# Kernel tuning notes

Measured on AMD Instinct MI355X. Metric: run time of the kernel, lower is better.

Reference implementation:

```python
import jax, jax.numpy as jnp
import numpy as np

EPS = 1e-6
N_HEAD = 16

def alibi_slopes(n_head):
    # standard ALiBi geometric slopes for power-of-2 head counts
    start = 2.0 ** (-8.0 / n_head)
    return (start ** np.arange(1, n_head + 1)).astype(np.float32)

def rsig(x):
    # rational sigmoid sigma(x) = 0.5 * (x / (|x| + 1) + 1)
    return 0.5 * (x / (jnp.abs(x) + 1.0) + 1.0)

def mr_norm(x, w):
    # RationalMR: x / (mean(|x|) + eps) * weight
    return x / (jnp.mean(jnp.abs(x), axis=-1, keepdims=True) + EPS) * w


def setup_inputs() -> dict:
    key = jax.random.key(0)
    ks = jax.random.split(key, 6)
    d_model, d_ffn = 1024, 4096
    B, T = 1, 2048
    x = jax.random.normal(ks[0], (B, T, d_model), dtype=jnp.float32)
    s = 0.02
    w_qkv = jax.random.normal(ks[1], (3 * d_model, d_model), dtype=jnp.float32) * s
    w_out = jax.random.normal(ks[2], (d_model, d_model), dtype=jnp.float32) * s
    w_merged = jax.random.normal(ks[3], (2 * d_ffn, d_model), dtype=jnp.float32) * s
    w3 = jax.random.normal(ks[4], (d_model, d_ffn), dtype=jnp.float32) * s
    norm1_w = jnp.ones((d_model,), dtype=jnp.float32)
    norm2_w = jnp.ones((d_model,), dtype=jnp.float32)
    return {"x": x, "w_qkv": w_qkv, "w_out": w_out, "w_merged": w_merged,
            "w3": w3, "norm1_w": norm1_w, "norm2_w": norm2_w}


def reference(x, w_qkv, w_out, w_merged, w3, norm1_w, norm2_w):
    B, T, C = x.shape
    H = N_HEAD
    D = C // H
    scale = 1.0 / jnp.sqrt(jnp.float32(D))

    # --- attention sub-block ---
    h = mr_norm(x, norm1_w)
    qkv = (h @ w_qkv.T).reshape(B, T, 3, H, D).transpose(2, 0, 3, 1, 4)  # [3,B,H,T,D]
    q, k, v = qkv[0], qkv[1], qkv[2]
    scores = jnp.einsum('bhtd,bhsd->bhts', q, k) * scale  # [B,H,T,T]
    pos = jnp.arange(T)
    rel = jnp.abs(pos[:, None] - pos[None, :]).astype(jnp.float32)
    slopes = jnp.asarray(alibi_slopes(H))
    scores = scores - rel[None, None] * slopes[None, :, None, None]
    causal = pos[None, :] > pos[:, None]  # mask j > i
    scores = jnp.where(causal[None, None], jnp.float32(-10000.0), scores)
    # rational softmax: sigma(s)^4 / (sum sigma(s)^4 + eps)
    p4 = rsig(scores) ** 4
    probs = p4 / (jnp.sum(p4, axis=-1, keepdims=True) + EPS)
    attn = jnp.einsum('bhts,bhsd->bhtd', probs, v)  # [B,H,T,D]
    attn = attn.transpose(0, 2, 1, 3).reshape(B, T, C)
    x = x + attn @ w_out.T

    # --- FFN sub-block (rational SwiGLU) ---
    h2 = mr_norm(x, norm2_w)
    merged = h2 @ w_merged.T
    gate, val = jnp.split(merged, 2, axis=-1)
    hidden = gate * rsig(gate) * val
    x = x + hidden @ w3.T
    return x
```

## Files before the change

### kernel.cpp

```cpp
#include <hip/hip_runtime.h>
#include <hip/hip_bf16.h>
#include <stdint.h>

typedef unsigned int u32;
typedef unsigned short u16;
typedef __attribute__((ext_vector_type(8))) short bf16x8;
typedef __attribute__((ext_vector_type(4))) float f32x4;

#define MFMA(a, b, c) __builtin_amdgcn_mfma_f32_16x16x32_bf16(a, b, c, 0, 0, 0)

__device__ __forceinline__ u16 f2bf(float f) {
  u32 u = __float_as_uint(f);
  return (u16)((u + 0x7FFFu + ((u >> 16) & 1u)) >> 16);
}
__device__ __forceinline__ float bf2f(u16 h) {
  return __uint_as_float(((u32)h) << 16);
}
__device__ __forceinline__ float rsig_fast(float sc) {
  return 0.5f + 0.5f * sc * __builtin_amdgcn_rcpf(fabsf(sc) + 1.f);
}
__device__ __forceinline__ void async16(void* lds, const void* g) {
  __builtin_amdgcn_global_load_lds((const __attribute__((address_space(1))) u32*)g,
                                   (__attribute__((address_space(3))) u32*)lds, 16, 0, 0);
}

__global__ __launch_bounds__(256) void to_bf16(const float* __restrict__ src,
                                               u16* __restrict__ dst) {
  const size_t i = (size_t)blockIdx.x * 256 + threadIdx.x;
  const float4 a = ((const float4*)src)[2 * i];
  const float4 b = ((const float4*)src)[2 * i + 1];
  ushort4 o0, o1;
  o0.x = f2bf(a.x); o0.y = f2bf(a.y); o0.z = f2bf(a.z); o0.w = f2bf(a.w);
  o1.x = f2bf(b.x); o1.y = f2bf(b.y); o1.z = f2bf(b.z); o1.w = f2bf(b.w);
  ((ushort4*)dst)[2 * i] = o0;
  ((ushort4*)dst)[2 * i + 1] = o1;
}

__global__ __launch_bounds__(256) void mrnorm(const float* __restrict__ x,
                                              const float* __restrict__ wg,
                                              u16* __restrict__ out) {
  const int row = blockIdx.x;
  const int tid = threadIdx.x;
  const float4 v = ((const float4*)(x + (size_t)row * 1024))[tid];
  float s = fabsf(v.x) + fabsf(v.y) + fabsf(v.z) + fabsf(v.w);
#pragma unroll
  for (int off = 1; off < 64; off <<= 1) s += __shfl_xor(s, off);
  __shared__ float red[4];
  if ((tid & 63) == 0) red[tid >> 6] = s;
  __syncthreads();
  const float inv = 1.f / ((red[0] + red[1] + red[2] + red[3]) * (1.f / 1024.f) + 1e-6f);
  const float4 g = ((const float4*)wg)[tid];
  ushort4 o;
  o.x = f2bf(v.x * inv * g.x);
  o.y = f2bf(v.y * inv * g.y);
  o.z = f2bf(v.z * inv * g.z);
  o.w = f2bf(v.w * inv * g.w);
  ((ushort4*)out)[(size_t)row * 256 + tid] = o;
}

template <int EPI, bool DBUF>
__global__ __launch_bounds__(256) void gemm_bt(const u16* __restrict__ A, int lda,
                                               const u16* __restrict__ B, int ldb,
                                               void* __restrict__ C,
                                               const float* __restrict__ resid,
                                               int M, int N, int K) {
  __shared__ __align__(16) u16 As[(DBUF ? 2 : 1) * 128 * 64];
  __shared__ __align__(16) u16 Bs[(DBUF ? 2 : 1) * 128 * 64];
  const int tid = threadIdx.x;
  const int lane = tid & 63;
  const int w = tid >> 6;
  const int wr = (w >> 1) << 6;
  const int wc = (w & 1) << 6;
  const int nbn = N >> 7;
  const int m0 = (blockIdx.x / nbn) << 7;
  const int n0 = (blockIdx.x % nbn) << 7;
  const int l15 = lane & 15;
  const int lhi = lane >> 4;
  A += (size_t)blockIdx.y * K;
  B += (size_t)blockIdx.y * K;

  f32x4 acc[4][4] = {};

  auto stage = [&](int buf, int k0) {
#pragma unroll
    for (int p = 0; p < 4; ++p) {
      const int c = p * 256 + tid;
      const int row = c >> 3;
      const int cb = (c & 7) << 4;
      const int src = cb ^ ((row & 7) << 4);
      async16((char*)As + buf * 16384 + c * 16,
              (const char*)A + ((size_t)(m0 + row) * lda + k0) * 2 + src);
      async16((char*)Bs + buf * 16384 + c * 16,
              (const char*)B + ((size_t)(n0 + row) * ldb + k0) * 2 + src);
    }
  };
  auto compute = [&](int buf) {
#pragma unroll
    for (int kk = 0; kk < 2; ++kk) {
      bf16x8 af[4], bfr[4];
#pragma unroll
      for (int m = 0; m < 4; ++m) {
        const int row = wr + (m << 4) + l15;
        const int off = row * 128 + (((kk << 6) + (lhi << 4)) ^ ((row & 7) << 4));
        af[m] = *(const bf16x8*)((const char*)As + buf * 16384 + off);
      }
#pragma unroll
      for (int n = 0; n < 4; ++n) {
        const int row = wc + (n << 4) + l15;
        const int off = row * 128 + (((kk << 6) + (lhi << 4)) ^ ((row & 7) << 4));
        bfr[n] = *(const bf16x8*)((const char*)Bs + buf * 16384 + off);
      }
#pragma unroll
      for (int m = 0; m < 4; ++m)
#pragma unroll
        for (int n = 0; n < 4; ++n)
          acc[m][n] = MFMA(af[m], bfr[n], acc[m][n]);
    }
  };

  if (DBUF) {
    stage(0, 0);
    __syncthreads();
    int cur = 0;
    for (int k0 = 0; k0 < K; k0 += 64) {
      if (k0 + 64 < K) stage(cur ^ 1, k0 + 64);
      compute(cur);
      __syncthreads();
      cur ^= 1;
    }
  } else {
    for (int k0 = 0; k0 < K; k0 += 64) {
      stage(0, k0);
      __syncthreads();
      compute(0);
      __syncthreads();
    }
  }

  u16* Cp = (u16*)C + (size_t)blockIdx.y * M * N;
#pragma unroll
  for (int m = 0; m < 4; ++m) {
#pragma unroll
    for (int n = 0; n < 4; ++n) {
      const int col = n0 + wc + (n << 4) + l15;
#pragma unroll
      for (int r = 0; r < 4; ++r) {
        const int row = m0 + wr + (m << 4) + (lhi << 2) + r;
        const float v = acc[m][n][r];
        if (EPI == 0) {
          Cp[(size_t)row * N + col] = f2bf(v);
        } else {
          const size_t idx = (size_t)row * N + col;
          ((float*)C)[idx] = resid[idx] + v;
        }
      }
    }
  }
}

__global__ __launch_bounds__(256) void splitk_reduce(const u16* __restrict__ part,
                                                     const float* __restrict__ resid,
                                                     float* __restrict__ out) {
  const size_t i = ((size_t)blockIdx.x * 256 + threadIdx.x) * 8;
  const float4 r0 = *(const float4*)(resid + i);
  const float4 r1 = *(const float4*)(resid + i + 4);
  float acc[8] = {r0.x, r0.y, r0.z, r0.w, r1.x, r1.y, r1.z, r1.w};
#pragma unroll
  for (int c = 0; c < 4; ++c) {
    const uint4 p = *(const uint4*)(part + (size_t)c * 2097152 + i);
    const u16* ps = (const u16*)&p;
#pragma unroll
    for (int j = 0; j < 8; ++j) acc[j] += bf2f(ps[j]);
  }
  float4 o0 = {acc[0], acc[1], acc[2], acc[3]};
  float4 o1 = {acc[4], acc[5], acc[6], acc[7]};
  *(float4*)(out + i) = o0;
  *(float4*)(out + i + 4) = o1;
}

__global__ __launch_bounds__(256) void transpose_v(const u16* __restrict__ qkv,
                                                   u16* __restrict__ vt) {
  __shared__ __align__(16) u16 tile[64][72];
  const int head = blockIdx.x >> 5;
  const int t0 = (blockIdx.x & 31) << 6;
  const int tid = threadIdx.x;
  const int row = tid >> 2;
  const int cb = (tid & 3) << 4;
  const u16* src = qkv + (size_t)(t0 + row) * 3072 + 2048 + head * 64 + cb;
  *(uint4*)&tile[row][cb] = *(const uint4*)src;
  *(uint4*)&tile[row][cb + 8] = *(const uint4*)(src + 8);
  __syncthreads();
  u16 buf[16];
#pragma unroll
  for (int j = 0; j < 16; ++j) buf[j] = tile[cb + j][row];
  u16* dst = vt + (size_t)(head * 64 + row) * 2048 + t0 + cb;
  *(uint4*)dst = *(const uint4*)&buf[0];
  *(uint4*)(dst + 8) = *(const uint4*)&buf[8];
}

__global__ __launch_bounds__(256) void attn_part(const u16* __restrict__ qkv,
                                                 const u16* __restrict__ vt,
                                                 u16* __restrict__ pnum,
                                                 float* __restrict__ pden) {
  const int id = blockIdx.x;
  const int head = id & 15;
  const int rem = id >> 4;
  int a, g;
  if (rem < 32)      { a = 3; g = rem; }
  else if (rem < 56) { a = 2; g = rem - 32; }
  else if (rem < 72) { a = 1; g = rem - 56; }
  else               { a = 0; g = rem - 72; }
  const int qb = (a << 3) + g / (a + 1);
  const int c = g - (g / (a + 1)) * (a + 1);
  const int slot = head * 80 + ((a * (a + 1)) << 2) + (qb - (a << 3)) * (a + 1) + c;

  __shared__ __align__(16) u16 Ks[2][64 * 64];
  __shared__ __align__(16) u16 Vs[2][64 * 64];
  __shared__ __align__(16) u16 QP[4][16 * 64];
  const int tid = threadIdx.x;
  const int lane = tid & 63;
  const int w = tid >> 6;
  const int l15 = lane & 15;
  const int lhi = lane >> 4;
  const int qbase = qb << 6;
  const float slope = exp2f(-0.5f * (float)(head + 1));

  auto stageKV = [&](int buf, int s0) {
#pragma unroll
    for (int p = 0; p < 2; ++p) {
      const int cc = p * 256 + tid;
      const int row = cc >> 3;
      const int cb = (cc & 7) << 4;
      const int src = cb ^ ((row & 7) << 4);
      async16((char*)Ks[buf] + cc * 16,
              (const char*)qkv + ((size_t)(s0 + row) * 3072 + 1024 + head * 64) * 2 + src);
      async16((char*)Vs[buf] + cc * 16,
              (const char*)vt + ((size_t)(head * 64 + row) * 2048 + s0) * 2 + src);
    }
  };

  const int sfirst = c << 9;
  const int smax = min(qbase, sfirst + 448);
#pragma unroll
  for (int p = 0; p < 2; ++p) {
    const int cc = p * 256 + tid;
    const int row = cc >> 3;
    const int cb = (cc & 7) << 4;
    const int src = cb ^ ((row & 7) << 4);
    async16((char*)QP + cc * 16,
            (const char*)qkv + ((size_t)(qbase + row) * 3072 + head * 64) * 2 + src);
  }
  stageKV(0, sfirst);
  __syncthreads();

  bf16x8 qf[2];
#pragma unroll
  for (int kk = 0; kk < 2; ++kk) {
    const int row = (w << 4) + l15;
    const int off = row * 128 + (((kk << 6) + (lhi << 4)) ^ ((row & 7) << 4));
    qf[kk] = *(const bf16x8*)((const char*)QP + off);
  }

  f32x4 oacc[4] = {};
  float rs[4] = {0.f, 0.f, 0.f, 0.f};
  u16* pw = (u16*)QP[w];
  int cur = 0;

  for (int s0 = sfirst; s0 <= smax; s0 += 64) {
    if (s0 + 64 <= smax) stageKV(cur ^ 1, s0 + 64);
    const char* Kc = (const char*)Ks[cur];
    const char* Vc = (const char*)Vs[cur];

    bf16x8 kf[4][2];
#pragma unroll
    for (int bb = 0; bb < 4; ++bb)
#pragma unroll
      for (int kk = 0; kk < 2; ++kk) {
        const int row = (bb << 4) + l15;
        const int off = row * 128 + (((kk << 6) + (lhi << 4)) ^ ((row & 7) << 4));
        kf[bb][kk] = *(const bf16x8*)(Kc + off);
      }
    f32x4 sa[4];
#pragma unroll
    for (int bb = 0; bb < 4; ++bb) {
      f32x4 z = {0.f, 0.f, 0.f, 0.f};
      z = MFMA(qf[0], kf[bb][0], z);
      sa[bb] = MFMA(qf[1], kf[bb][1], z);
    }
#pragma unroll
    for (int bb = 0; bb < 4; ++bb) {
      const int s_abs = s0 + (bb << 4) + l15;
#pragma unroll
      for (int r = 0; r < 4; ++r) {
        const int prow = (lhi << 2) + r;
        const int q_abs = qbase + (w << 4) + prow;
        float p4 = 0.f;
        if (s_abs <= q_abs) {
          const float sc = sa[bb][r] * 0.125f - slope * (float)(q_abs - s_abs);
          const float t = rsig_fast(sc);
          const float t2 = t * t;
          p4 = t2 * t2;
        }
        rs[r] += p4;
        const int pcol2 = ((bb << 4) + l15) << 1;
        const int poff = prow * 128 + (pcol2 ^ ((prow & 7) << 4));
        *(u16*)((char*)pw + poff) = f2bf(p4);
      }
    }
    bf16x8 pf[2];
#pragma unroll
    for (int kk = 0; kk < 2; ++kk) {
      const int row = l15;
      const int off = row * 128 + (((kk << 6) + (lhi << 4)) ^ ((row & 7) << 4));
      pf[kk] = *(const bf16x8*)((const char*)pw + off);
    }
#pragma unroll
    for (int db = 0; db < 4; ++db) {
#pragma unroll
      for (int kk = 0; kk < 2; ++kk) {
        const int row = (db << 4) + l15;
        const int off = row * 128 + (((kk << 6) + (lhi << 4)) ^ ((row & 7) << 4));
        const bf16x8 vf = *(const bf16x8*)(Vc + off);
        oacc[db] = MFMA(pf[kk], vf, oacc[db]);
      }
    }
    __syncthreads();
    cur ^= 1;
  }

#pragma unroll
  for (int r = 0; r < 4; ++r) {
    float v = rs[r];
    v += __shfl_xor(v, 1);
    v += __shfl_xor(v, 2);
    v += __shfl_xor(v, 4);
    v += __shfl_xor(v, 8);
    rs[r] = v;
  }
  if (l15 == 0) {
#pragma unroll
    for (int r = 0; r < 4; ++r)
      pden[(size_t)slot * 64 + (w << 4) + (lhi << 2) + r] = rs[r];
  }
  __syncthreads();
#pragma unroll
  for (int db = 0; db < 4; ++db)
#pragma unroll
    for (int r = 0; r < 4; ++r)
      pw[((lhi << 2) + r) * 64 + (db << 4) + l15] = f2bf(oacc[db][r]);
  __syncthreads();
  {
    const int row = lane >> 2;
    const int cb = (lane & 3) << 4;
    const u16* s = pw + row * 64 + cb;
    const uint4 d0 = *(const uint4*)s;
    const uint4 d1 = *(const uint4*)(s + 8);
    u16* dst = pnum + (size_t)slot * 4096 + ((w << 4) + row) * 64 + cb;
    *(uint4*)dst = d0;
    *(uint4*)(dst + 8) = d1;
  }
}

__global__ __launch_bounds__(256) void attn_merge(const u16* __restrict__ pnum,
                                                  const float* __restrict__ pden,
                                                  u16* __restrict__ out) {
  const int head = blockIdx.x >> 5;
  const int qb = blockIdx.x & 31;
  const int nc = (qb >> 3) + 1;
  const int a = qb >> 3, b = qb & 7;
  const int slot0 = head * 80 + ((a * (a + 1)) << 2) + b * (a + 1);
  const int tid = threadIdx.x;
  const int row = tid >> 2;
  const int c0 = (tid & 3) << 4;

  float acc[16] = {};
  float den = 0.f;
  for (int ci = 0; ci < nc; ++ci) {
    const int slot = slot0 + ci;
    den += pden[(size_t)slot * 64 + row];
    const u16* np = pnum + (size_t)slot * 4096 + row * 64 + c0;
    const uint4 n0 = *(const uint4*)np;
    const uint4 n1 = *(const uint4*)(np + 8);
    const u16* ns0 = (const u16*)&n0;
    const u16* ns1 = (const u16*)&n1;
#pragma unroll
    for (int j = 0; j < 8; ++j) {
      acc[j] += bf2f(ns0[j]);
      acc[8 + j] += bf2f(ns1[j]);
    }
  }
  const float inv = 1.f / (den + 1e-6f);
  u16 ob[16];
#pragma unroll
  for (int j = 0; j < 16; ++j) ob[j] = f2bf(acc[j] * inv);
  u16* dst = out + (size_t)((qb << 6) + row) * 1024 + head * 64 + c0;
  *(uint4*)dst = *(const uint4*)&ob[0];
  *(uint4*)(dst + 8) = *(const uint4*)&ob[8];
}

__global__ __launch_bounds__(256) void swiglu(u16* __restrict__ merged) {
  const size_t i = (size_t)blockIdx.x * 256 + threadIdx.x;
  const int t = (int)(i >> 9);
  const int f = (int)(i & 511) << 3;
  u16* gp = merged + (size_t)t * 8192 + f;
  const uint4 gu = *(const uint4*)gp;
  const uint4 vu = *(const uint4*)(gp + 4096);
  const u16* gs = (const u16*)&gu;
  const u16* vs = (const u16*)&vu;
  u16 ob[8];
#pragma unroll
  for (int j = 0; j < 8; ++j) {
    const float gv = bf2f(gs[j]);
    const float vv = bf2f(vs[j]);
    ob[j] = f2bf(gv * rsig_fast(gv) * vv);
  }
  *(uint4*)gp = *(const uint4*)ob;
}

extern "C" void kernel_launch(void* const* d_in, const int* in_sizes, int n_in,
                              void* d_out, int out_size, void* d_ws, size_t ws_size,
                              hipStream_t stream) {
  const float* x     = (const float*)d_in[0];
  const float* wqkv  = (const float*)d_in[1];
  const float* wout  = (const float*)d_in[2];
  const float* wmer  = (const float*)d_in[3];
  const float* w3    = (const float*)d_in[4];
  const float* n1w   = (const float*)d_in[5];
  const float* n2w   = (const float*)d_in[6];
  char* ws = (char*)d_ws;

  u16*   WQKV = (u16*)(ws + 0);
  u16*   WOUT = (u16*)(ws + 6291456);
  u16*   WMER = (u16*)(ws + 8388608);
  u16*   W3B  = (u16*)(ws + 25165824);
  float* X1   = (float*)(ws + 33554432);
  u16*   QKV  = (u16*)(ws + 41943040);
  u16*   VT   = (u16*)(ws + 54525952);
  u16*   ATTN = (u16*)(ws + 58720256);
  u16*   PNUM = (u16*)(ws + 62914560);
  float* PDEN = (float*)(ws + 73400320);
  u16*   MER  = (u16*)(ws + 41943040);
  u16*   PART = (u16*)(ws + 8388608);
  u16*   H    = (u16*)(ws + 75497472);
  u16*   H2   = (u16*)(ws + 75497472);

  to_bf16<<<1536, 256, 0, stream>>>(wqkv, WQKV);
  to_bf16<<<512, 256, 0, stream>>>(wout, WOUT);
  to_bf16<<<4096, 256, 0, stream>>>(wmer, WMER);
  to_bf16<<<2048, 256, 0, stream>>>(w3, W3B);

  mrnorm<<<2048, 256, 0, stream>>>(x, n1w, H);
  gemm_bt<0, true><<<16 * 24, 256, 0, stream>>>(H, 1024, WQKV, 1024, QKV, nullptr,
                                                2048, 3072, 1024);
  transpose_v<<<512, 256, 0, stream>>>(QKV, VT);
  attn_part<<<1280, 256, 0, stream>>>(QKV, VT, PNUM, PDEN);
  attn_merge<<<512, 256, 0, stream>>>(PNUM, PDEN, ATTN);
  gemm_bt<1, true><<<16 * 8, 256, 0, stream>>>(ATTN, 1024, WOUT, 1024, X1, x,
                                               2048, 1024, 1024);

  mrnorm<<<2048, 256, 0, stream>>>(X1, n2w, H2);
  gemm_bt<0, false><<<16 * 64, 256, 0, stream>>>(H2, 1024, WMER, 1024, MER, nullptr,
                                                 2048, 8192, 1024);
  swiglu<<<4096, 256, 0, stream>>>(MER);
  gemm_bt<0, true><<<dim3(16 * 8, 4), 256, 0, stream>>>(MER, 8192, W3B, 4096, PART,
                                                        nullptr, 2048, 1024, 1024);
  splitk_reduce<<<1024, 256, 0, stream>>>(PART, X1, (float*)d_out);
}
```

Measured before the change: 201.4 us.

## Fuse SwiGLU into the FFN up-projection GEMM with paired gate/value tiles

Adds a dedicated GEMM kernel that computes matching gate and value output tiles in one block, keeping both accumulator sets in registers and applying the rational SwiGLU in the epilogue. This removes the separate swiglu pass and the write and re-read of the full 2048x8192 merged tensor. The down-projection now reads a compact 4096-wide hidden buffer. In exchange, the kernel doubles its accumulator registers and LDS for B tiles, which may lower occupancy. It also drops whatever pipelining or tuning the generic gemm_bt had.

Measured after the change: 200.9 us. About the same (-0.2%).

```diff
diff --git a/kernel.cpp b/kernel.cpp
--- a/kernel.cpp
+++ b/kernel.cpp
@@ -158,6 +158,80 @@
   }
 }
 
+__global__ __launch_bounds__(256) void gemm_ffn1(const u16* __restrict__ A,
+                                                 const u16* __restrict__ B,
+                                                 u16* __restrict__ hid) {
+  __shared__ __align__(16) u16 As[128 * 64];
+  __shared__ __align__(16) u16 Bg[128 * 64];
+  __shared__ __align__(16) u16 Bv[128 * 64];
+  const int tid = threadIdx.x;
+  const int lane = tid & 63;
+  const int w = tid >> 6;
+  const int wr = (w >> 1) << 6;
+  const int wc = (w & 1) << 6;
+  const int m0 = (blockIdx.x >> 5) << 7;
+  const int n0 = (blockIdx.x & 31) << 7;
+  const int l15 = lane & 15;
+  const int lhi = lane >> 4;
+
+  f32x4 ag[4][4] = {};
+  f32x4 av[4][4] = {};
+
+  for (int k0 = 0; k0 < 1024; k0 += 64) {
+#pragma unroll
+    for (int p = 0; p < 4; ++p) {
+      const int c = p * 256 + tid;
+      const int row = c >> 3;
+      const int cb = (c & 7) << 4;
+      const int src = cb ^ ((row & 7) << 4);
+      async16((char*)As + c * 16, (const char*)A + ((size_t)(m0 + row) * 1024 + k0) * 2 + src);
+      async16((char*)Bg + c * 16, (const char*)B + ((size_t)(n0 + row) * 1024 + k0) * 2 + src);
+      async16((char*)Bv + c * 16, (const char*)B + ((size_t)(4096 + n0 + row) * 1024 + k0) * 2 + src);
+    }
+    __syncthreads();
+#pragma unroll
+    for (int kk = 0; kk < 2; ++kk) {
+      bf16x8 af[4], bg[4], bv[4];
+#pragma unroll
+      for (int m = 0; m < 4; ++m) {
+        const int row = wr + (m << 4) + l15;
+        const int off = row * 128 + (((kk << 6) + (lhi << 4)) ^ ((row & 7) << 4));
+        af[m] = *(const bf16x8*)((const char*)As + off);
+      }
+#pragma unroll
+      for (int n = 0; n < 4; ++n) {
+        const int row = wc + (n << 4) + l15;
+        const int off = row * 128 + (((kk << 6) + (lhi << 4)) ^ ((row & 7) << 4));
+        bg[n] = *(const bf16x8*)((const char*)Bg + off);
+        bv[n] = *(const bf16x8*)((const char*)Bv + off);
+      }
+#pragma unroll
+      for (int m = 0; m < 4; ++m)
+#pragma unroll
+        for (int n = 0; n < 4; ++n) {
+          ag[m][n] = MFMA(af[m], bg[n], ag[m][n]);
+          av[m][n] = MFMA(af[m], bv[n], av[m][n]);
+        }
+    }
+    __syncthreads();
+  }
+
+#pragma unroll
+  for (int m = 0; m < 4; ++m) {
+#pragma unroll
+    for (int n = 0; n < 4; ++n) {
+      const int col = n0 + wc + (n << 4) + l15;
+#pragma unroll
+      for (int r = 0; r < 4; ++r) {
+        const int row = m0 + wr + (m << 4) + (lhi << 2) + r;
+        const float g = ag[m][n][r];
+        const float v = av[m][n][r];
+        hid[(size_t)row * 4096 + col] = f2bf(g * rsig_fast(g) * v);
+      }
+    }
+  }
+}
+
 __global__ __launch_bounds__(256) void splitk_reduce(const u16* __restrict__ part,
                                                      const float* __restrict__ resid,
                                                      float* __restrict__ out) {
@@ -398,25 +472,6 @@
   *(uint4*)(dst + 8) = *(const uint4*)&ob[8];
 }
 
-__global__ __launch_bounds__(256) void swiglu(u16* __restrict__ merged) {
-  const size_t i = (size_t)blockIdx.x * 256 + threadIdx.x;
-  const int t = (int)(i >> 9);
-  const int f = (int)(i & 511) << 3;
-  u16* gp = merged + (size_t)t * 8192 + f;
-  const uint4 gu = *(const uint4*)gp;
-  const uint4 vu = *(const uint4*)(gp + 4096);
-  const u16* gs = (const u16*)&gu;
-  const u16* vs = (const u16*)&vu;
-  u16 ob[8];
-#pragma unroll
-  for (int j = 0; j < 8; ++j) {
-    const float gv = bf2f(gs[j]);
-    const float vv = bf2f(vs[j]);
-    ob[j] = f2bf(gv * rsig_fast(gv) * vv);
-  }
-  *(uint4*)gp = *(const uint4*)ob;
-}
-
 extern "C" void kernel_launch(void* const* d_in, const int* in_sizes, int n_in,
                               void* d_out, int out_size, void* d_ws, size_t ws_size,
                               hipStream_t stream) {
@@ -439,7 +494,7 @@
   u16*   ATTN = (u16*)(ws + 58720256);
   u16*   PNUM = (u16*)(ws + 62914560);
   float* PDEN = (float*)(ws + 73400320);
-  u16*   MER  = (u16*)(ws + 41943040);
+  u16*   HID  = (u16*)(ws + 41943040);
   u16*   PART = (u16*)(ws + 8388608);
   u16*   H    = (u16*)(ws + 75497472);
   u16*   H2   = (u16*)(ws + 75497472);
@@ -459,10 +514,8 @@
                                                2048, 1024, 1024);
 
   mrnorm<<<2048, 256, 0, stream>>>(X1, n2w, H2);
-  gemm_bt<0, false><<<16 * 64, 256, 0, stream>>>(H2, 1024, WMER, 1024, MER, nullptr,
-                                                 2048, 8192, 1024);
-  swiglu<<<4096, 256, 0, stream>>>(MER);
-  gemm_bt<0, true><<<dim3(16 * 8, 4), 256, 0, stream>>>(MER, 8192, W3B, 4096, PART,
+  gemm_ffn1<<<512, 256, 0, stream>>>(H2, WMER, HID);
+  gemm_bt<0, true><<<dim3(16 * 8, 4), 256, 0, stream>>>(HID, 4096, W3B, 4096, PART,
                                                         nullptr, 2048, 1024, 1024);
   splitk_reduce<<<1024, 256, 0, stream>>>(PART, X1, (float*)d_out);
 }
```
